# Performance work log

Hardware: AMD Instinct MI355X
Metric: run time of the kernel (lower is better)

The kernel has to match this reference:

```python
import jax, jax.numpy as jnp
import numpy as np

D_MODEL = 1024
NUM_HEADS = 16
D_K = D_MODEL // NUM_HEADS
TEMPERATURE = 1.0
EPS = 1e-6


def setup_inputs() -> dict:
    key = jax.random.key(0)
    ks = jax.random.split(key, 8)
    B, S, D, H = 2, 2048, D_MODEL, NUM_HEADS
    sc = 1.0 / np.sqrt(D)
    x = jax.random.normal(ks[0], (B, S, D), dtype=jnp.float32)
    Wq = jax.random.normal(ks[1], (D, D), dtype=jnp.float32) * sc
    Wk = jax.random.normal(ks[2], (D, D), dtype=jnp.float32) * sc
    Wv = jax.random.normal(ks[3], (D, D), dtype=jnp.float32) * sc
    Wo = jax.random.normal(ks[4], (D, D), dtype=jnp.float32) * sc
    bo = jnp.zeros((D,), dtype=jnp.float32)
    phase_scale = jnp.ones((H,), dtype=jnp.float32)
    # orthogonal init for entanglement matrix
    q, _ = np.linalg.qr(np.random.default_rng(0).normal(size=(H, H)))
    ent = jnp.asarray(q, dtype=jnp.float32)
    gamma = jnp.ones((D,), dtype=jnp.float32)
    beta = jnp.zeros((D,), dtype=jnp.float32)
    return {"x": x, "Wq": Wq, "Wk": Wk, "Wv": Wv, "Wo": Wo, "bo": bo,
            "phase_scale": phase_scale, "ent": ent, "gamma": gamma, "beta": beta}


def reference(x, Wq, Wk, Wv, Wo, bo, phase_scale, ent, gamma, beta):
    B, S, D = x.shape
    H, dk = NUM_HEADS, D_K
    # projections -> [B, H, S, dk]
    Q = (x @ Wq).reshape(B, S, H, dk).transpose(0, 2, 1, 3)
    K = (x @ Wk).reshape(B, S, H, dk).transpose(0, 2, 1, 3)
    V = (x @ Wv).reshape(B, S, H, dk).transpose(0, 2, 1, 3)
    # per-head QK^T, scaled, phase-modulated
    scores = jnp.einsum('bhqd,bhkd->bhqk', Q, K)
    inv = 1.0 / (float(np.sqrt(dk)) * TEMPERATURE)
    s = scores * (inv * phase_scale)[None, :, None, None]
    # real part of quantum phase: cos(s) + 0.1*cos(2s)  (imag part of V is zero,
    # so head_output = attended_real; the 0.1*attended_imag term vanishes)
    w = jnp.cos(s) + 0.1 * jnp.cos(2.0 * s)
    w = jax.nn.softmax(w, axis=-1)
    att = jnp.einsum('bhqk,bhkd->bhqd', w, V).transpose(0, 2, 1, 3)  # [B,S,H,dk]
    # faithful reproduction of tf.einsum('bsnd,hm->bsmd', ...): sums over n AND h
    att = jnp.einsum('bsnd,hm->bsmd', att, ent)
    out = att.reshape(B, S, D) @ Wo + bo
    r = out + x
    mu = jnp.mean(r, axis=-1, keepdims=True)
    var = jnp.mean(jnp.square(r - mu), axis=-1, keepdims=True)
    return gamma * (r - mu) * jax.lax.rsqrt(var + EPS) + beta
```

## Files before the change

### kernel.cpp

```cpp
#include <hip/hip_runtime.h>
#include <cstdint>
#include <cstddef>

#define S_LEN 2048
#define DMODEL 1024
#define NHEADS 16
#define DKH 64
#define MROWS 4096
#define BH_CNT 32

typedef __bf16 bf16x8 __attribute__((ext_vector_type(8)));
typedef __bf16 bf16x2 __attribute__((ext_vector_type(2)));
typedef float f32x4 __attribute__((ext_vector_type(4)));
typedef unsigned int u32x4 __attribute__((ext_vector_type(4)));
typedef unsigned int u32;
typedef unsigned short u16;

__device__ __forceinline__ u16 f2bfu(float f) {
  u32 u = __float_as_uint(f);
  return (u16)((u + 0x7FFFu + ((u >> 16) & 1u)) >> 16);
}

__device__ __forceinline__ float bf2f(u16 v) {
  return __uint_as_float((u32)v << 16);
}

__device__ __forceinline__ u32 pk_bf16(float a, float b) {
  bf16x2 v;
  v[0] = (__bf16)a;
  v[1] = (__bf16)b;
  return __builtin_bit_cast(u32, v);
}

__device__ __forceinline__ void pl32swap(u32& a, u32& b) {
#if __has_builtin(__builtin_amdgcn_permlane32_swap)
  auto r = __builtin_amdgcn_permlane32_swap((int)a, (int)b, false, false);
  a = (u32)r[0]; b = (u32)r[1];
#else
  asm volatile("v_permlane32_swap_b32 %0, %1" : "+v"(a), "+v"(b));
#endif
}
__device__ __forceinline__ void pl16swap(u32& a, u32& b) {
#if __has_builtin(__builtin_amdgcn_permlane16_swap)
  auto r = __builtin_amdgcn_permlane16_swap((int)a, (int)b, false, false);
  a = (u32)r[0]; b = (u32)r[1];
#else
  asm volatile("v_permlane16_swap_b32 %0, %1" : "+v"(a), "+v"(b));
#endif
}

__device__ __forceinline__ void gload16(void* lds, const void* g) {
  __builtin_amdgcn_global_load_lds(
      (const __attribute__((address_space(1))) void*)g,
      (__attribute__((address_space(3))) void*)lds, 16, 0, 0);
}

__global__ __launch_bounds__(256) void prep_all_k(const float* __restrict__ x,
    const float* __restrict__ Wq, const float* __restrict__ Wk,
    const float* __restrict__ Wv, const float* __restrict__ Wo,
    const float* __restrict__ ps, const float* __restrict__ ent,
    u16* __restrict__ xb, u16* __restrict__ Wb, float* __restrict__ Woeff) {
  __shared__ float tile[32][33];
  int bid = blockIdx.x;
  int t = threadIdx.x;
  if (bid < 4096) {
    int i = (bid * 256 + t) * 4;
    float4 v = *(const float4*)(x + i);
    *(uint2*)(xb + i) = make_uint2(pk_bf16(v.x, v.y), pk_bf16(v.z, v.w));
  } else if (bid < 7168) {
    int lb = bid - 4096;
    int sel = lb >> 10, rem = lb & 1023;
    int k0 = (rem & 31) * 32, c0 = (rem >> 5) * 32;
    const float* W = sel == 0 ? Wq : (sel == 1 ? Wk : Wv);
    int tx = t & 31, ty = t >> 5;
#pragma unroll
    for (int i = 0; i < 4; ++i)
      tile[ty + i * 8][tx] = W[(size_t)(k0 + ty + i * 8) * DMODEL + c0 + tx];
    __syncthreads();
#pragma unroll
    for (int i = 0; i < 4; ++i) {
      int row = ty + i * 8;
      float v = tile[tx][row];
      if (sel == 1) v *= 0.019894367886486918f * ps[(c0 + row) >> 6];
      Wb[(size_t)(sel * 1024 + c0 + row) * DMODEL + k0 + tx] = f2bfu(v);
    }
  } else {
    __shared__ float e[16];
    if (t < 16) {
      float s = 0.f;
#pragma unroll
      for (int h = 0; h < 16; ++h) s += ent[h * 16 + t];
      e[t] = s;
    }
    __syncthreads();
    int gid = (bid - 7168) * 256 + t;
    int d = gid >> 10, j = gid & 1023;
    float acc = 0.f;
#pragma unroll
    for (int m = 0; m < 16; ++m) acc += e[m] * Wo[(size_t)((m << 6) + d) * DMODEL + j];
    Woeff[(size_t)d * DMODEL + j] = acc;
  }
}

__global__ __launch_bounds__(256) void gemm_qkv_k(const u16* __restrict__ xb,
    const u16* __restrict__ Wb, u16* __restrict__ Qb, u16* __restrict__ Kb,
    u16* __restrict__ Vt) {
  __shared__ __align__(16) u16 SMEM[2][2][128 * 32];
  int bid = blockIdx.x;
  int xcd = bid & 7, wi = bid >> 3;
  int mg = xcd >> 1, ng = xcd & 1;
  int mt = mg * 8 + (wi & 7);
  int nt = ng * 12 + (wi >> 3);
  int m0 = mt * 128, n0 = nt * 128;
  int tid = threadIdx.x;
  int lane = tid & 63, w = tid >> 6;
  int c = lane & 15, g = lane >> 4;
  int wr = w >> 1, wc = w & 1;

  int cij0 = (w * 2) * 64 + lane, cij1 = (w * 2 + 1) * 64 + lane;
  int row0 = cij0 >> 2, kp0 = (cij0 & 3) ^ (row0 & 3);
  int row1 = cij1 >> 2, kp1 = (cij1 & 3) ^ (row1 & 3);
  const u16* a0p = xb + (size_t)(m0 + row0) * DMODEL + kp0 * 8;
  const u16* a1p = xb + (size_t)(m0 + row1) * DMODEL + kp1 * 8;
  const u16* b0p = Wb + (size_t)(n0 + row0) * DMODEL + kp0 * 8;
  const u16* b1p = Wb + (size_t)(n0 + row1) * DMODEL + kp1 * 8;

  f32x4 acc[4][4];
#pragma unroll
  for (int i = 0; i < 4; ++i)
#pragma unroll
    for (int j = 0; j < 4; ++j) acc[i][j] = (f32x4){0.f, 0.f, 0.f, 0.f};

  gload16(&SMEM[0][0][(w * 2) * 512], a0p);
  gload16(&SMEM[0][0][(w * 2 + 1) * 512], a1p);
  gload16(&SMEM[1][0][(w * 2) * 512], b0p);
  gload16(&SMEM[1][0][(w * 2 + 1) * 512], b1p);
  __syncthreads();

  int cur = 0;
  for (int kt = 0; kt < DMODEL; kt += 32) {
    if (kt + 32 < DMODEL) {
      int nx = cur ^ 1, ko = kt + 32;
      gload16(&SMEM[0][nx][(w * 2) * 512], a0p + ko);
      gload16(&SMEM[0][nx][(w * 2 + 1) * 512], a1p + ko);
      gload16(&SMEM[1][nx][(w * 2) * 512], b0p + ko);
      gload16(&SMEM[1][nx][(w * 2 + 1) * 512], b1p + ko);
    }
    const u16* Ac = SMEM[0][cur];
    const u16* Bc = SMEM[1][cur];
    bf16x8 af[4], bf[4];
#pragma unroll
    for (int i = 0; i < 4; ++i) {
      int ra = wr * 64 + i * 16 + c;
      af[i] = *(const bf16x8*)(Ac + ra * 32 + ((g ^ (ra & 3)) * 8));
      int rb = wc * 64 + i * 16 + c;
      bf[i] = *(const bf16x8*)(Bc + rb * 32 + ((g ^ (rb & 3)) * 8));
    }
#pragma unroll
    for (int i = 0; i < 4; ++i)
#pragma unroll
      for (int j = 0; j < 4; ++j)
        acc[i][j] = __builtin_amdgcn_mfma_f32_16x16x32_bf16(af[i], bf[j], acc[i][j], 0, 0, 0);
    __syncthreads();
    cur ^= 1;
  }

  int sel = n0 >> 10;
  char* Ls = (char*)&SMEM[0][0][0];
  if (sel == 2) {
#pragma unroll
    for (int i = 0; i < 4; ++i)
#pragma unroll
      for (int jf = 0; jf < 4; ++jf) {
        int n = wc * 64 + jf * 16 + c;
        int m = wr * 64 + i * 16 + 4 * g;
        int byte = n * 256 + ((m * 2) ^ ((n & 7) << 4));
        *(uint2*)(Ls + byte) = make_uint2(pk_bf16(acc[i][jf][0], acc[i][jf][1]),
                                          pk_bf16(acc[i][jf][2], acc[i][jf][3]));
      }
  } else {
#pragma unroll
    for (int i = 0; i < 4; ++i)
#pragma unroll
      for (int jf = 0; jf < 4; ++jf) {
        int n = wc * 64 + jf * 16 + c;
#pragma unroll
        for (int j = 0; j < 4; ++j) {
          int m = wr * 64 + i * 16 + 4 * g + j;
          int byte = m * 256 + ((n * 2) ^ ((m & 7) << 4));
          __bf16 hv = (__bf16)acc[i][jf][j];
          *(u16*)(Ls + byte) = __builtin_bit_cast(u16, hv);
        }
      }
  }
  __syncthreads();
  int r = tid >> 1, half = tid & 1;
  int h0 = (n0 & 1023) >> 6;
  int b = m0 >> 11, sbase = m0 & 2047;
  u16* dst;
  if (sel == 2) {
    int bh = b * 16 + h0 + (r >> 6), d = r & 63;
    dst = Vt + ((size_t)bh * DKH + d) * S_LEN + sbase + half * 64;
  } else {
    u16* base = (sel == 0 ? Qb : Kb);
    int bh = b * 16 + h0 + half;
    dst = base + ((size_t)bh * S_LEN + sbase + r) * DKH;
  }
#pragma unroll
  for (int kk = 0; kk < 8; ++kk) {
    int byte = r * 256 + ((half * 128 + kk * 16) ^ ((r & 7) << 4));
    *(uint4*)(dst + kk * 8) = *(const uint4*)(Ls + byte);
  }
}

__global__ __launch_bounds__(512) void attn_k(const u16* __restrict__ Qb,
    const u16* __restrict__ Kb, const u16* __restrict__ Vt,
    u16* __restrict__ attbufb) {
  __shared__ __align__(16) u16 Ks[4][4096];
  __shared__ __align__(16) u16 Vs[4][4096];
  __shared__ float dred[8][2][16];
  int fid = blockIdx.x;
  int swz = (fid & 7) * 64 + (fid >> 3);
  int bh = swz >> 4, qb = swz & 15;
  int tid = threadIdx.x;
  int lane = tid & 63, w = tid >> 6;
  int c = lane & 15, g = lane >> 4;
  int grp = w >> 2, h = (w >> 1) & 1, qh = w & 1;
  int q0 = qb * 128 + grp * 64;
  const float L2E = 1.4426950408889634f;

  const u16* Kbase = Kb + (size_t)bh * S_LEN * DKH;
  const u16* Vbase = Vt + (size_t)bh * DKH * S_LEN;

  int srow = w * 8 + (lane >> 3), slot = lane & 7, kp = slot ^ (srow & 7);
  const u16* kSrc = Kbase + (size_t)srow * DKH + kp * 8;
  const u16* vSrc = Vbase + (size_t)srow * S_LEN + kp * 8;
  auto stage = [&](int buf, int tile) {
    gload16(&Ks[buf][w * 512], kSrc + (size_t)tile * 64 * DKH);
    gload16(&Vs[buf][w * 512], vSrc + tile * 64);
  };

  int rot = qb * 2;
  stage(0, rot & 31);
  stage(1, (rot + 1) & 31);

  bf16x8 qf[2][2];
#pragma unroll
  for (int qg = 0; qg < 2; ++qg) {
    const u16* qp = Qb + ((size_t)bh * S_LEN + q0 + qh * 32 + qg * 16 + c) * DKH + g * 8;
    qf[qg][0] = *(const bf16x8*)qp;
    qf[qg][1] = *(const bf16x8*)(qp + 32);
  }
  bf16x8 onesf;
#pragma unroll
  for (int i = 0; i < 8; ++i) onesf[i] = (__bf16)1.0f;

  const u16* kptr[2][2];
#pragma unroll
  for (int fm = 0; fm < 2; ++fm) {
    int row = h * 32 + fm * 16 + c;
    kptr[fm][0] = &Ks[0][row * 64 + ((g ^ (row & 7)) * 8)];
    kptr[fm][1] = &Ks[0][row * 64 + (((4 + g) ^ (row & 7)) * 8)];
  }
  const u16* vptr[4];
#pragma unroll
  for (int fd = 0; fd < 4; ++fd) {
    int vrow = fd * 16 + c;
    vptr[fd] = &Vs[0][vrow * 64 + (((4 * h + g) ^ (vrow & 7)) * 8)];
  }

  f32x4 attT[4][2];
#pragma unroll
  for (int i = 0; i < 4; ++i)
#pragma unroll
    for (int qg = 0; qg < 2; ++qg) attT[i][qg] = (f32x4){0.f, 0.f, 0.f, 0.f};
  f32x4 denacc[2];
  denacc[0] = (f32x4){0.f, 0.f, 0.f, 0.f};
  denacc[1] = (f32x4){0.f, 0.f, 0.f, 0.f};

  auto compute = [&](const int off) {
    f32x4 sT[2][2];
    __builtin_amdgcn_s_setprio(1);
#pragma unroll
    for (int fm = 0; fm < 2; ++fm) {
      bf16x8 a0 = *(const bf16x8*)(kptr[fm][0] + off);
      bf16x8 a1 = *(const bf16x8*)(kptr[fm][1] + off);
#pragma unroll
      for (int qg = 0; qg < 2; ++qg) {
        f32x4 z = (f32x4){0.f, 0.f, 0.f, 0.f};
        z = __builtin_amdgcn_mfma_f32_16x16x32_bf16(a0, qf[qg][0], z, 0, 0, 0);
        sT[fm][qg] = __builtin_amdgcn_mfma_f32_16x16x32_bf16(a1, qf[qg][1], z, 0, 0, 0);
      }
    }
    __builtin_amdgcn_s_setprio(0);
    u32 wq[2][2][2];
#pragma unroll
    for (int fm = 0; fm < 2; ++fm)
#pragma unroll
      for (int qg = 0; qg < 2; ++qg) {
        float pv[4];
#pragma unroll
        for (int j = 0; j < 4; ++j) {
          float cv = __builtin_amdgcn_cosf(sT[fm][qg][j]);
          float w2 = __fmaf_rn(cv, __fmaf_rn(0.2f * L2E, cv, L2E), -0.1f * L2E);
          pv[j] = __builtin_amdgcn_exp2f(w2);
        }
        wq[qg][fm][0] = pk_bf16(pv[0], pv[1]);
        wq[qg][fm][1] = pk_bf16(pv[2], pv[3]);
      }
    bf16x8 pf[2];
#pragma unroll
    for (int qg = 0; qg < 2; ++qg) {
      u32 b0 = wq[qg][0][0], b2 = wq[qg][1][0];
      pl32swap(b0, b2);
      pl16swap(b0, b2);
      u32 b1 = wq[qg][0][1], b3 = wq[qg][1][1];
      pl32swap(b1, b3);
      pl16swap(b1, b3);
      pf[qg] = __builtin_bit_cast(bf16x8, (u32x4){b0, b1, b2, b3});
    }
    __builtin_amdgcn_s_setprio(1);
#pragma unroll
    for (int fd = 0; fd < 4; ++fd) {
      bf16x8 vf = *(const bf16x8*)(vptr[fd] + off);
#pragma unroll
      for (int qg = 0; qg < 2; ++qg)
        attT[fd][qg] = __builtin_amdgcn_mfma_f32_16x16x32_bf16(vf, pf[qg], attT[fd][qg], 0, 0, 0);
    }
#pragma unroll
    for (int qg = 0; qg < 2; ++qg)
      denacc[qg] = __builtin_amdgcn_mfma_f32_16x16x32_bf16(onesf, pf[qg], denacc[qg], 0, 0, 0);
    __builtin_amdgcn_s_setprio(0);
  };

  __syncthreads();
  for (int t = 0; t < 32; t += 4) {
    stage(2, (t + 2 + rot) & 31);
    stage(3, (t + 3 + rot) & 31);
    compute(0);
    compute(4096);
    __syncthreads();
    if (t + 4 < 32) {
      stage(0, (t + 4 + rot) & 31);
      stage(1, (t + 5 + rot) & 31);
    }
    compute(8192);
    compute(12288);
    __syncthreads();
  }

  if (g == 0) {
    dred[w][0][c] = denacc[0][0];
    dred[w][1][c] = denacc[1][0];
  }
  float* Rq = (grp ? (float*)&Vs[0][0] : (float*)&Ks[0][0]) + qh * 2048;
  if (h == 1) {
#pragma unroll
    for (int fd = 0; fd < 4; ++fd)
#pragma unroll
      for (int qg = 0; qg < 2; ++qg)
        *(f32x4*)&Rq[(qg * 16 + c) * 64 + fd * 16 + 4 * g] = attT[fd][qg];
  }
  __syncthreads();
  if (h == 0) {
    float inv[2];
#pragma unroll
    for (int qg = 0; qg < 2; ++qg)
      inv[qg] = 1.f / (dred[w][qg][c] + dred[w ^ 2][qg][c]);
#pragma unroll
    for (int fd = 0; fd < 4; ++fd)
#pragma unroll
      for (int qg = 0; qg < 2; ++qg) {
        f32x4 part = *(const f32x4*)&Rq[(qg * 16 + c) * 64 + fd * 16 + 4 * g];
        f32x4 tot = (attT[fd][qg] + part) * inv[qg];
        int q = q0 + qh * 32 + qg * 16 + c;
        *(uint2*)(attbufb + ((size_t)bh * S_LEN + q) * DKH + fd * 16 + 4 * g) =
            make_uint2(pk_bf16(tot[0], tot[1]), pk_bf16(tot[2], tot[3]));
      }
  }
}

__global__ __launch_bounds__(256) void fuse_out_ln_k(const u16* __restrict__ attbufb,
    const float* __restrict__ Woeff, const float* __restrict__ bo,
    const float* __restrict__ x, const float* __restrict__ gamma,
    const float* __restrict__ beta, float* __restrict__ out) {
  __shared__ float red[8][256];
  __shared__ __align__(16) float a[8][64];
  __shared__ float sred[8][4][2];
  int t = threadIdx.x;
  int r0 = blockIdx.x * 8;
  int d = t & 63, hg = t >> 6;
#pragma unroll
  for (int rr = 0; rr < 8; ++rr) {
    int m = r0 + rr, b = m >> 11, sr = m & 2047;
    float pa = 0.f;
#pragma unroll
    for (int hh = 0; hh < 4; ++hh) {
      int h = hg * 4 + hh;
      pa += bf2f(attbufb[(((size_t)(b * 16 + h)) * S_LEN + sr) * DKH + d]);
    }
    red[rr][t] = pa;
  }
  __syncthreads();
#pragma unroll
  for (int e = 0; e < 2; ++e) {
    int idx = t + e * 256;
    int rr = idx >> 6, dd = idx & 63;
    a[rr][dd] = red[rr][dd] + red[rr][64 + dd] + red[rr][128 + dd] + red[rr][192 + dd];
  }
  __syncthreads();

  float o[8][4];
#pragma unroll
  for (int rr = 0; rr < 8; ++rr) { o[rr][0] = o[rr][1] = o[rr][2] = o[rr][3] = 0.f; }
  int c4 = t * 4;
  for (int dd = 0; dd < 64; dd += 4) {
    float4 wv0 = *(const float4*)(Woeff + (size_t)(dd + 0) * DMODEL + c4);
    float4 wv1 = *(const float4*)(Woeff + (size_t)(dd + 1) * DMODEL + c4);
    float4 wv2 = *(const float4*)(Woeff + (size_t)(dd + 2) * DMODEL + c4);
    float4 wv3 = *(const float4*)(Woeff + (size_t)(dd + 3) * DMODEL + c4);
#pragma unroll
    for (int rr = 0; rr < 8; ++rr) {
      float4 av = *(const float4*)&a[rr][dd];
      o[rr][0] += av.x * wv0.x + av.y * wv1.x + av.z * wv2.x + av.w * wv3.x;
      o[rr][1] += av.x * wv0.y + av.y * wv1.y + av.z * wv2.y + av.w * wv3.y;
      o[rr][2] += av.x * wv0.z + av.y * wv1.z + av.z * wv2.z + av.w * wv3.z;
      o[rr][3] += av.x * wv0.w + av.y * wv1.w + av.z * wv2.w + av.w * wv3.w;
    }
  }
  float4 bv = *(const float4*)(bo + c4);
  int w = t >> 6, lane = t & 63;
#pragma unroll
  for (int rr = 0; rr < 8; ++rr) {
    int m = r0 + rr;
    float4 xv = *(const float4*)(x + (size_t)m * DMODEL + c4);
    o[rr][0] += bv.x + xv.x;
    o[rr][1] += bv.y + xv.y;
    o[rr][2] += bv.z + xv.z;
    o[rr][3] += bv.w + xv.w;
    float s = o[rr][0] + o[rr][1] + o[rr][2] + o[rr][3];
    float q = o[rr][0] * o[rr][0] + o[rr][1] * o[rr][1] + o[rr][2] * o[rr][2] + o[rr][3] * o[rr][3];
#pragma unroll
    for (int mm = 1; mm < 64; mm <<= 1) {
      s += __shfl_xor(s, mm, 64);
      q += __shfl_xor(q, mm, 64);
    }
    if (lane == 0) { sred[rr][w][0] = s; sred[rr][w][1] = q; }
  }
  __syncthreads();
  float4 gv = *(const float4*)(gamma + c4);
  float4 bev = *(const float4*)(beta + c4);
#pragma unroll
  for (int rr = 0; rr < 8; ++rr) {
    float s = sred[rr][0][0] + sred[rr][1][0] + sred[rr][2][0] + sred[rr][3][0];
    float q = sred[rr][0][1] + sred[rr][1][1] + sred[rr][2][1] + sred[rr][3][1];
    float mu = s * (1.f / 1024.f);
    float var = q * (1.f / 1024.f) - mu * mu;
    float rs = rsqrtf(var + 1e-6f);
    int m = r0 + rr;
    float4 ov;
    ov.x = gv.x * (o[rr][0] - mu) * rs + bev.x;
    ov.y = gv.y * (o[rr][1] - mu) * rs + bev.y;
    ov.z = gv.z * (o[rr][2] - mu) * rs + bev.z;
    ov.w = gv.w * (o[rr][3] - mu) * rs + bev.w;
    *(float4*)(out + (size_t)m * DMODEL + c4) = ov;
  }
}

extern "C" void kernel_launch(void* const* d_in, const int* in_sizes, int n_in,
                              void* d_out, int out_size, void* d_ws, size_t ws_size,
                              hipStream_t stream) {
  const float* x = (const float*)d_in[0];
  const float* Wq = (const float*)d_in[1];
  const float* Wk = (const float*)d_in[2];
  const float* Wv = (const float*)d_in[3];
  const float* Wo = (const float*)d_in[4];
  const float* bo = (const float*)d_in[5];
  const float* ps = (const float*)d_in[6];
  const float* ent = (const float*)d_in[7];
  const float* gamma = (const float*)d_in[8];
  const float* beta = (const float*)d_in[9];
  float* out = (float*)d_out;

  char* ws = (char*)d_ws;
  size_t o = 0;
  u16* xb = (u16*)(ws + o);    o += (size_t)MROWS * DMODEL * 2;
  u16* Wb = (u16*)(ws + o);    o += (size_t)3072 * 1024 * 2;
  u16* Qb = (u16*)(ws + o);    o += (size_t)BH_CNT * S_LEN * DKH * 2;
  u16* Kb = (u16*)(ws + o);    o += (size_t)BH_CNT * S_LEN * DKH * 2;
  u16* Vt = (u16*)(ws + o);    o += (size_t)BH_CNT * S_LEN * DKH * 2;
  float* Woeff = (float*)(ws + o);   o += (size_t)DKH * DMODEL * 4;
  u16* attbufb = (u16*)(ws + o);     o += (size_t)BH_CNT * S_LEN * DKH * 2;

  prep_all_k<<<dim3(7424), dim3(256), 0, stream>>>(x, Wq, Wk, Wv, Wo, ps, ent,
                                                   xb, Wb, Woeff);
  gemm_qkv_k<<<dim3(768), dim3(256), 0, stream>>>(xb, Wb, Qb, Kb, Vt);
  attn_k<<<dim3(512), dim3(512), 0, stream>>>(Qb, Kb, Vt, attbufb);
  fuse_out_ln_k<<<dim3(512), dim3(256), 0, stream>>>(attbufb, Woeff, bo, x, gamma, beta, out);
}
```

Baseline: 123.7 us.

## Split attention key range across two blocks and combine partial sums later

Each attention block now covers only half of the key sequence, so the grid doubles from 512 to 1024 blocks and shared-memory staging drops to double buffering. The unnormalized partial outputs and partial softmax denominators go to doubled workspace buffers, and the output/LayerNorm kernel adds the two halves and normalizes. This is meant to raise occupancy and balance load on the GPU, since 512 blocks underfill it. The cost is more global traffic for the doubled partial buffers, an extra denominator read, and a second bf16 rounding of the unnormalized partials.

```diff
diff --git a/kernel.cpp b/kernel.cpp
--- a/kernel.cpp
+++ b/kernel.cpp
@@ -215,13 +215,14 @@
 
 __global__ __launch_bounds__(512) void attn_k(const u16* __restrict__ Qb,
     const u16* __restrict__ Kb, const u16* __restrict__ Vt,
-    u16* __restrict__ attbufb) {
-  __shared__ __align__(16) u16 Ks[4][4096];
-  __shared__ __align__(16) u16 Vs[4][4096];
+    u16* __restrict__ attbufb, float* __restrict__ dpart) {
+  __shared__ __align__(16) u16 Ks[2][4096];
+  __shared__ __align__(16) u16 Vs[2][4096];
   __shared__ float dred[8][2][16];
   int fid = blockIdx.x;
-  int swz = (fid & 7) * 64 + (fid >> 3);
-  int bh = swz >> 4, qb = swz & 15;
+  int swz = (fid & 7) * 128 + (fid >> 3);
+  int bh = swz >> 5, rem = swz & 31;
+  int qb = rem >> 1, kh = rem & 1;
   int tid = threadIdx.x;
   int lane = tid & 63, w = tid >> 6;
   int c = lane & 15, g = lane >> 4;
@@ -229,8 +230,8 @@
   int q0 = qb * 128 + grp * 64;
   const float L2E = 1.4426950408889634f;
 
-  const u16* Kbase = Kb + (size_t)bh * S_LEN * DKH;
-  const u16* Vbase = Vt + (size_t)bh * DKH * S_LEN;
+  const u16* Kbase = Kb + (size_t)bh * S_LEN * DKH + (size_t)(kh * 1024) * DKH;
+  const u16* Vbase = Vt + (size_t)bh * DKH * S_LEN + kh * 1024;
 
   int srow = w * 8 + (lane >> 3), slot = lane & 7, kp = slot ^ (srow & 7);
   const u16* kSrc = Kbase + (size_t)srow * DKH + kp * 8;
@@ -240,9 +241,8 @@
     gload16(&Vs[buf][w * 512], vSrc + tile * 64);
   };
 
-  int rot = qb * 2;
-  stage(0, rot & 31);
-  stage(1, (rot + 1) & 31);
+  int rot = qb & 15;
+  stage(0, rot);
 
   bf16x8 qf[2][2];
 #pragma unroll
@@ -334,18 +334,12 @@
   };
 
   __syncthreads();
-  for (int t = 0; t < 32; t += 4) {
-    stage(2, (t + 2 + rot) & 31);
-    stage(3, (t + 3 + rot) & 31);
+  for (int t = 0; t < 16; t += 2) {
+    stage(1, (t + 1 + rot) & 15);
     compute(0);
+    __syncthreads();
+    if (t + 2 < 16) stage(0, (t + 2 + rot) & 15);
     compute(4096);
-    __syncthreads();
-    if (t + 4 < 32) {
-      stage(0, (t + 4 + rot) & 31);
-      stage(1, (t + 5 + rot) & 31);
-    }
-    compute(8192);
-    compute(12288);
     __syncthreads();
   }
 
@@ -363,27 +357,32 @@
   }
   __syncthreads();
   if (h == 0) {
-    float inv[2];
-#pragma unroll
-    for (int qg = 0; qg < 2; ++qg)
-      inv[qg] = 1.f / (dred[w][qg][c] + dred[w ^ 2][qg][c]);
+    float den0 = dred[w][0][c] + dred[w ^ 2][0][c];
+    float den1 = dred[w][1][c] + dred[w ^ 2][1][c];
+    u16* ob = attbufb + (size_t)(kh * BH_CNT + bh) * S_LEN * DKH;
 #pragma unroll
     for (int fd = 0; fd < 4; ++fd)
 #pragma unroll
       for (int qg = 0; qg < 2; ++qg) {
         f32x4 part = *(const f32x4*)&Rq[(qg * 16 + c) * 64 + fd * 16 + 4 * g];
-        f32x4 tot = (attT[fd][qg] + part) * inv[qg];
+        f32x4 tot = attT[fd][qg] + part;
         int q = q0 + qh * 32 + qg * 16 + c;
-        *(uint2*)(attbufb + ((size_t)bh * S_LEN + q) * DKH + fd * 16 + 4 * g) =
+        *(uint2*)(ob + (size_t)q * DKH + fd * 16 + 4 * g) =
             make_uint2(pk_bf16(tot[0], tot[1]), pk_bf16(tot[2], tot[3]));
       }
+    if (g == 0) {
+      float* dp = dpart + (size_t)(kh * BH_CNT + bh) * S_LEN;
+      dp[q0 + qh * 32 + c] = den0;
+      dp[q0 + qh * 32 + 16 + c] = den1;
+    }
   }
 }
 
 __global__ __launch_bounds__(256) void fuse_out_ln_k(const u16* __restrict__ attbufb,
-    const float* __restrict__ Woeff, const float* __restrict__ bo,
-    const float* __restrict__ x, const float* __restrict__ gamma,
-    const float* __restrict__ beta, float* __restrict__ out) {
+    const float* __restrict__ dpart, const float* __restrict__ Woeff,
+    const float* __restrict__ bo, const float* __restrict__ x,
+    const float* __restrict__ gamma, const float* __restrict__ beta,
+    float* __restrict__ out) {
   __shared__ float red[8][256];
   __shared__ __align__(16) float a[8][64];
   __shared__ float sred[8][4][2];
@@ -396,8 +395,14 @@
     float pa = 0.f;
 #pragma unroll
     for (int hh = 0; hh < 4; ++hh) {
-      int h = hg * 4 + hh;
-      pa += bf2f(attbufb[(((size_t)(b * 16 + h)) * S_LEN + sr) * DKH + d]);
+      int hidx = b * 16 + hg * 4 + hh;
+      size_t o1 = (size_t)hidx * S_LEN + sr;
+      size_t o2 = (size_t)(BH_CNT + hidx) * S_LEN + sr;
+      float dn = dpart[o1] + dpart[o2];
+      float inv = 1.f / dn;
+      float v1 = bf2f(attbufb[o1 * DKH + d]);
+      float v2 = bf2f(attbufb[o2 * DKH + d]);
+      pa += (v1 + v2) * inv;
     }
     red[rr][t] = pa;
   }
@@ -490,11 +495,13 @@
   u16* Kb = (u16*)(ws + o);    o += (size_t)BH_CNT * S_LEN * DKH * 2;
   u16* Vt = (u16*)(ws + o);    o += (size_t)BH_CNT * S_LEN * DKH * 2;
   float* Woeff = (float*)(ws + o);   o += (size_t)DKH * DMODEL * 4;
-  u16* attbufb = (u16*)(ws + o);     o += (size_t)BH_CNT * S_LEN * DKH * 2;
+  u16* attbufb = (u16*)(ws + o);     o += (size_t)2 * BH_CNT * S_LEN * DKH * 2;
+  float* dpart = (float*)(ws + o);   o += (size_t)2 * BH_CNT * S_LEN * 4;
 
   prep_all_k<<<dim3(7424), dim3(256), 0, stream>>>(x, Wq, Wk, Wv, Wo, ps, ent,
                                                    xb, Wb, Woeff);
   gemm_qkv_k<<<dim3(768), dim3(256), 0, stream>>>(xb, Wb, Qb, Kb, Vt);
-  attn_k<<<dim3(512), dim3(512), 0, stream>>>(Qb, Kb, Vt, attbufb);
-  fuse_out_ln_k<<<dim3(512), dim3(256), 0, stream>>>(attbufb, Woeff, bo, x, gamma, beta, out);
-}
+  attn_k<<<dim3(1024), dim3(512), 0, stream>>>(Qb, Kb, Vt, attbufb, dpart);
+  fuse_out_ln_k<<<dim3(512), dim3(256), 0, stream>>>(attbufb, dpart, Woeff, bo, x,
+                                                     gamma, beta, out);
+}
```

Result: slower. 128.0 us (+3.5%).

## Enlarge QKV GEMM tiles to 256x256 with 512-thread blocks

Applied to the files above, without the earlier changes.

Reworks the QKV projection GEMM from 128x128 tiles on 256 threads to 256x256 tiles on 512 threads, with each wave computing a 128x64 sub-tile. The main loop is unrolled by two k-steps with a double-buffered LDS stage, and the epilogue writes the two M halves in turn through shared memory. The aim is more data reuse per loaded tile and less global traffic. The cost is only 192 blocks, fewer than one per CU on a 256-CU part, plus higher register pressure from 32 accumulators.

```diff
diff --git a/kernel.cpp b/kernel.cpp
--- a/kernel.cpp
+++ b/kernel.cpp
@@ -102,114 +102,122 @@
   }
 }
 
-__global__ __launch_bounds__(256) void gemm_qkv_k(const u16* __restrict__ xb,
+__global__ __launch_bounds__(512, 2) void gemm_qkv_k(const u16* __restrict__ xb,
     const u16* __restrict__ Wb, u16* __restrict__ Qb, u16* __restrict__ Kb,
     u16* __restrict__ Vt) {
-  __shared__ __align__(16) u16 SMEM[2][2][128 * 32];
+  __shared__ __align__(16) u16 As[2][8192];
+  __shared__ __align__(16) u16 Bs[2][8192];
   int bid = blockIdx.x;
   int xcd = bid & 7, wi = bid >> 3;
-  int mg = xcd >> 1, ng = xcd & 1;
-  int mt = mg * 8 + (wi & 7);
-  int nt = ng * 12 + (wi >> 3);
-  int m0 = mt * 128, n0 = nt * 128;
+  int mt = (xcd >> 1) * 4 + (wi & 3);
+  int nt = (xcd & 1) * 6 + (wi >> 2);
+  int m0 = mt * 256, n0 = nt * 256;
   int tid = threadIdx.x;
   int lane = tid & 63, w = tid >> 6;
   int c = lane & 15, g = lane >> 4;
-  int wr = w >> 1, wc = w & 1;
-
-  int cij0 = (w * 2) * 64 + lane, cij1 = (w * 2 + 1) * 64 + lane;
-  int row0 = cij0 >> 2, kp0 = (cij0 & 3) ^ (row0 & 3);
-  int row1 = cij1 >> 2, kp1 = (cij1 & 3) ^ (row1 & 3);
-  const u16* a0p = xb + (size_t)(m0 + row0) * DMODEL + kp0 * 8;
-  const u16* a1p = xb + (size_t)(m0 + row1) * DMODEL + kp1 * 8;
-  const u16* b0p = Wb + (size_t)(n0 + row0) * DMODEL + kp0 * 8;
-  const u16* b1p = Wb + (size_t)(n0 + row1) * DMODEL + kp1 * 8;
-
-  f32x4 acc[4][4];
-#pragma unroll
-  for (int i = 0; i < 4; ++i)
+  int wr = w >> 2, wcn = w & 3;
+
+  int r2 = tid >> 2, s2 = tid & 3;
+  const u16* aS = xb + (size_t)(m0 + r2) * DMODEL + ((s2 ^ (r2 & 3)) * 8);
+  const u16* bS = Wb + (size_t)(n0 + r2) * DMODEL + ((s2 ^ (r2 & 3)) * 8);
+
+  int xorc = (g ^ (c & 3)) * 8;
+  int aoff[8], boff[4];
+#pragma unroll
+  for (int mf = 0; mf < 8; ++mf) aoff[mf] = (wr * 128 + mf * 16 + c) * 32 + xorc;
+#pragma unroll
+  for (int nf = 0; nf < 4; ++nf) boff[nf] = (wcn * 64 + nf * 16 + c) * 32 + xorc;
+
+  f32x4 acc[8][4];
+#pragma unroll
+  for (int i = 0; i < 8; ++i)
 #pragma unroll
     for (int j = 0; j < 4; ++j) acc[i][j] = (f32x4){0.f, 0.f, 0.f, 0.f};
 
-  gload16(&SMEM[0][0][(w * 2) * 512], a0p);
-  gload16(&SMEM[0][0][(w * 2 + 1) * 512], a1p);
-  gload16(&SMEM[1][0][(w * 2) * 512], b0p);
-  gload16(&SMEM[1][0][(w * 2 + 1) * 512], b1p);
+  auto stage = [&](int buf, int kt) {
+    gload16(&As[buf][tid * 8], aS + kt);
+    gload16(&As[buf][4096 + tid * 8], aS + 128 * DMODEL + kt);
+    gload16(&Bs[buf][tid * 8], bS + kt);
+    gload16(&Bs[buf][4096 + tid * 8], bS + 128 * DMODEL + kt);
+  };
+  auto compute = [&](const int off) {
+    bf16x8 bfr[4];
+#pragma unroll
+    for (int nf = 0; nf < 4; ++nf) bfr[nf] = *(const bf16x8*)(&Bs[0][0] + off + boff[nf]);
+#pragma unroll
+    for (int mf = 0; mf < 8; ++mf) {
+      bf16x8 af = *(const bf16x8*)(&As[0][0] + off + aoff[mf]);
+#pragma unroll
+      for (int nf = 0; nf < 4; ++nf)
+        acc[mf][nf] = __builtin_amdgcn_mfma_f32_16x16x32_bf16(af, bfr[nf], acc[mf][nf], 0, 0, 0);
+    }
+  };
+
+  stage(0, 0);
   __syncthreads();
-
-  int cur = 0;
-  for (int kt = 0; kt < DMODEL; kt += 32) {
-    if (kt + 32 < DMODEL) {
-      int nx = cur ^ 1, ko = kt + 32;
-      gload16(&SMEM[0][nx][(w * 2) * 512], a0p + ko);
-      gload16(&SMEM[0][nx][(w * 2 + 1) * 512], a1p + ko);
-      gload16(&SMEM[1][nx][(w * 2) * 512], b0p + ko);
-      gload16(&SMEM[1][nx][(w * 2 + 1) * 512], b1p + ko);
-    }
-    const u16* Ac = SMEM[0][cur];
-    const u16* Bc = SMEM[1][cur];
-    bf16x8 af[4], bf[4];
-#pragma unroll
-    for (int i = 0; i < 4; ++i) {
-      int ra = wr * 64 + i * 16 + c;
-      af[i] = *(const bf16x8*)(Ac + ra * 32 + ((g ^ (ra & 3)) * 8));
-      int rb = wc * 64 + i * 16 + c;
-      bf[i] = *(const bf16x8*)(Bc + rb * 32 + ((g ^ (rb & 3)) * 8));
-    }
-#pragma unroll
-    for (int i = 0; i < 4; ++i)
-#pragma unroll
-      for (int j = 0; j < 4; ++j)
-        acc[i][j] = __builtin_amdgcn_mfma_f32_16x16x32_bf16(af[i], bf[j], acc[i][j], 0, 0, 0);
-    __syncthreads();
-    cur ^= 1;
-  }
-
-  int sel = n0 >> 10;
-  char* Ls = (char*)&SMEM[0][0][0];
-  if (sel == 2) {
-#pragma unroll
-    for (int i = 0; i < 4; ++i)
-#pragma unroll
-      for (int jf = 0; jf < 4; ++jf) {
-        int n = wc * 64 + jf * 16 + c;
-        int m = wr * 64 + i * 16 + 4 * g;
-        int byte = n * 256 + ((m * 2) ^ ((n & 7) << 4));
-        *(uint2*)(Ls + byte) = make_uint2(pk_bf16(acc[i][jf][0], acc[i][jf][1]),
-                                          pk_bf16(acc[i][jf][2], acc[i][jf][3]));
+  for (int kt = 0; kt < DMODEL; kt += 64) {
+    stage(1, kt + 32);
+    compute(0);
+    __syncthreads();
+    if (kt + 64 < DMODEL) stage(0, kt + 64);
+    compute(8192);
+    __syncthreads();
+  }
+
+  int sel = nt >> 2;
+  int h0 = (nt & 3) * 4;
+  int b = m0 >> 11, sbase = m0 & 2047;
+  char* Ls = (char*)&As[0][0];
+#pragma unroll
+  for (int half = 0; half < 2; ++half) {
+    if (wr == half) {
+      if (sel == 2) {
+#pragma unroll
+        for (int mf = 0; mf < 8; ++mf)
+#pragma unroll
+          for (int nf = 0; nf < 4; ++nf) {
+            int n = wcn * 64 + nf * 16 + c;
+            int mh = mf * 16 + 4 * g;
+            *(uint2*)(Ls + n * 256 + ((mh * 2) ^ ((n & 7) << 4))) =
+                make_uint2(pk_bf16(acc[mf][nf][0], acc[mf][nf][1]),
+                           pk_bf16(acc[mf][nf][2], acc[mf][nf][3]));
+          }
+      } else {
+#pragma unroll
+        for (int mf = 0; mf < 8; ++mf)
+#pragma unroll
+          for (int nf = 0; nf < 4; ++nf) {
+            int n = wcn * 64 + nf * 16 + c;
+#pragma unroll
+            for (int j = 0; j < 4; ++j) {
+              int mh = mf * 16 + 4 * g + j;
+              __bf16 hv = (__bf16)acc[mf][nf][j];
+              *(u16*)(Ls + mh * 512 + ((n * 2) ^ ((mh & 7) << 4))) =
+                  __builtin_bit_cast(u16, hv);
+            }
+          }
       }
-  } else {
-#pragma unroll
-    for (int i = 0; i < 4; ++i)
-#pragma unroll
-      for (int jf = 0; jf < 4; ++jf) {
-        int n = wc * 64 + jf * 16 + c;
-#pragma unroll
-        for (int j = 0; j < 4; ++j) {
-          int m = wr * 64 + i * 16 + 4 * g + j;
-          int byte = m * 256 + ((n * 2) ^ ((m & 7) << 4));
-          __bf16 hv = (__bf16)acc[i][jf][j];
-          *(u16*)(Ls + byte) = __builtin_bit_cast(u16, hv);
-        }
-      }
-  }
-  __syncthreads();
-  int r = tid >> 1, half = tid & 1;
-  int h0 = (n0 & 1023) >> 6;
-  int b = m0 >> 11, sbase = m0 & 2047;
-  u16* dst;
-  if (sel == 2) {
-    int bh = b * 16 + h0 + (r >> 6), d = r & 63;
-    dst = Vt + ((size_t)bh * DKH + d) * S_LEN + sbase + half * 64;
-  } else {
-    u16* base = (sel == 0 ? Qb : Kb);
-    int bh = b * 16 + h0 + half;
-    dst = base + ((size_t)bh * S_LEN + sbase + r) * DKH;
-  }
-#pragma unroll
-  for (int kk = 0; kk < 8; ++kk) {
-    int byte = r * 256 + ((half * 128 + kk * 16) ^ ((r & 7) << 4));
-    *(uint4*)(dst + kk * 8) = *(const uint4*)(Ls + byte);
+    }
+    __syncthreads();
+    if (sel == 2) {
+      int n = tid >> 1, cc = tid & 1;
+      int head = h0 + (n >> 6), d = n & 63;
+      u16* dst = Vt + ((size_t)(b * 16 + head) * DKH + d) * S_LEN + sbase + half * 128 + cc * 64;
+#pragma unroll
+      for (int kk = 0; kk < 8; ++kk)
+        *(uint4*)(dst + kk * 8) =
+            *(const uint4*)(Ls + n * 256 + ((cc * 128 + kk * 16) ^ ((n & 7) << 4)));
+    } else {
+      int r = tid >> 2, cc = tid & 3;
+      int head = h0 + cc;
+      u16* base = (sel == 0 ? Qb : Kb);
+      u16* dst = base + ((size_t)(b * 16 + head) * S_LEN + sbase + half * 128 + r) * DKH;
+#pragma unroll
+      for (int kk = 0; kk < 8; ++kk)
+        *(uint4*)(dst + kk * 8) =
+            *(const uint4*)(Ls + r * 512 + ((cc * 128 + kk * 16) ^ ((r & 7) << 4)));
+    }
+    __syncthreads();
   }
 }
 
@@ -494,7 +502,7 @@
 
   prep_all_k<<<dim3(7424), dim3(256), 0, stream>>>(x, Wq, Wk, Wv, Wo, ps, ent,
                                                    xb, Wb, Woeff);
-  gemm_qkv_k<<<dim3(768), dim3(256), 0, stream>>>(xb, Wb, Qb, Kb, Vt);
+  gemm_qkv_k<<<dim3(192), dim3(512), 0, stream>>>(xb, Wb, Qb, Kb, Vt);
   attn_k<<<dim3(512), dim3(512), 0, stream>>>(Qb, Kb, Vt, attbufb);
   fuse_out_ln_k<<<dim3(512), dim3(256), 0, stream>>>(attbufb, Woeff, bo, x, gamma, beta, out);
 }
```

Result: no change. 123.8 us (+0.1%).
